# Optimization experiments

Hardware: AMD Instinct MI355X
Metric: run time of the kernel (lower is better)

The kernel has to match this reference:

```python
import jax, jax.numpy as jnp
import numpy as np

EPSILON_BASE = 0.1
N_ITERS = 10


def setup_inputs() -> dict:
    key = jax.random.key(0)
    k1, k2 = jax.random.split(key)
    N, D = 8192, 512
    embeddings = jax.random.normal(k1, (N, D), dtype=jnp.float32)
    target_noise = jax.random.normal(k2, (N, D), dtype=jnp.float32)
    return {"embeddings": embeddings, "target_noise": target_noise}


def _l2_normalize(x, axis=1, eps=1e-12):
    # matches torch.nn.functional.normalize (divide by max(norm, eps))
    norm = jnp.sqrt(jnp.sum(x * x, axis=axis, keepdims=True))
    return x / jnp.maximum(norm, eps)


def _sinkhorn(x, y):
    n, d = x.shape
    # normalize_embeddings=True path
    x = _l2_normalize(x, axis=1)
    y = _l2_normalize(y, axis=1)
    epsilon = EPSILON_BASE * 2.0
    # squared euclidean cost: C[i,j] = ||x_i - y_j||^2  (cdist p=2, squared)
    sq_x = jnp.sum(x * x, axis=1, keepdims=True)          # (n,1)
    sq_y = jnp.sum(y * y, axis=1, keepdims=True)          # (n,1)
    C = jnp.maximum(sq_x + sq_y.T - 2.0 * (x @ y.T), 0.0)  # (n,n)
    log_K = -C / epsilon

    def body(carry, _):
        log_u, log_v = carry
        log_u = -jax.nn.logsumexp(log_K + log_v[None, :], axis=1)
        log_v = -jax.nn.logsumexp(log_K.T + log_u[None, :], axis=1)
        return (log_u, log_v), None

    init = (jnp.zeros(n, dtype=x.dtype), jnp.zeros(n, dtype=y.dtype))
    (log_u, log_v), _ = jax.lax.scan(body, init, None, length=N_ITERS)

    log_P = log_u[:, None] + log_K + log_v[None, :]
    P = jnp.clip(jnp.exp(log_P), 0.0, 1.0)
    distance = jnp.sum(P * C) / n

    # nan/inf fallback: 1 - mean cosine similarity (x, y already unit norm)
    fallback = 1.0 - jnp.mean(jnp.sum(x * y, axis=1))
    bad = jnp.isnan(distance) | jnp.isinf(distance)
    return jnp.where(bad, fallback, distance)


def reference(embeddings, target_noise):
    if embeddings.ndim == 3:
        embeddings = embeddings.reshape(-1, embeddings.shape[-1])
        target_noise = target_noise.reshape(-1, target_noise.shape[-1])
    return _sinkhorn(embeddings, target_noise)
```

## Files before the change

kernel.cpp:

```cpp
#include <hip/hip_runtime.h>
#include <hip/hip_bf16.h>
#include <hip/hip_fp16.h>
#include <stdint.h>

#define NROW 8192
#define DIM  512
#define LN2   0.6931471805599453f
#define TEN_LOG2E 14.426950408889634f

typedef __attribute__((ext_vector_type(8))) short short8;
typedef __attribute__((ext_vector_type(4))) float f32x4;
typedef __attribute__((ext_vector_type(2))) float f32x2;

#define GLL16(gp, lp) __builtin_amdgcn_global_load_lds( \
    (const __attribute__((address_space(1))) void*)(gp), \
    (__attribute__((address_space(3))) void*)(lp), 16, 0, 0)

__device__ __forceinline__ float block_sum256(float v) {
  #pragma unroll
  for (int off = 32; off > 0; off >>= 1) v += __shfl_down(v, off, 64);
  __shared__ float sb[4];
  const int w = threadIdx.x >> 6;
  if ((threadIdx.x & 63) == 0) sb[w] = v;
  __syncthreads();
  return sb[0] + sb[1] + sb[2] + sb[3];
}

__global__ __launch_bounds__(256) void init_kernel(float* __restrict__ colrcp,
                                                   float* __restrict__ diagacc,
                                                   float* __restrict__ distacc) {
  const int g = blockIdx.x * 256 + threadIdx.x;
  colrcp[g] = 1.0f;
  if (g == 0) { diagacc[0] = 0.f; distacc[0] = 0.f; }
}

__global__ __launch_bounds__(256) void normalize_kernel(
    const float* __restrict__ X, const float* __restrict__ Y,
    __hip_bfloat16* __restrict__ Xn, __hip_bfloat16* __restrict__ Yn,
    float* __restrict__ diagacc) {
  const int wave = threadIdx.x >> 6, lane = threadIdx.x & 63;
  float dsum = 0.f;
  #pragma unroll
  for (int rr = 0; rr < 4; rr++) {
    const int row = blockIdx.x * 16 + wave * 4 + rr;
    const float4* xr = (const float4*)(X + (size_t)row * DIM);
    const float4* yr = (const float4*)(Y + (size_t)row * DIM);
    float4 x0 = xr[lane], x1 = xr[lane + 64];
    float4 y0 = yr[lane], y1 = yr[lane + 64];
    float sx = x0.x*x0.x + x0.y*x0.y + x0.z*x0.z + x0.w*x0.w
             + x1.x*x1.x + x1.y*x1.y + x1.z*x1.z + x1.w*x1.w;
    float sy = y0.x*y0.x + y0.y*y0.y + y0.z*y0.z + y0.w*y0.w
             + y1.x*y1.x + y1.y*y1.y + y1.z*y1.z + y1.w*y1.w;
    float sxy = x0.x*y0.x + x0.y*y0.y + x0.z*y0.z + x0.w*y0.w
              + x1.x*y1.x + x1.y*y1.y + x1.z*y1.z + x1.w*y1.w;
    #pragma unroll
    for (int off = 1; off < 64; off <<= 1) {
      sx  += __shfl_xor(sx, off, 64);
      sy  += __shfl_xor(sy, off, 64);
      sxy += __shfl_xor(sxy, off, 64);
    }
    const float rx = 1.0f / fmaxf(sqrtf(sx), 1e-12f);
    const float ry = 1.0f / fmaxf(sqrtf(sy), 1e-12f);
    if (lane == 0) dsum += sxy * rx * ry;
    ushort4 px, py;
    { __hip_bfloat16 b;
      b = __float2bfloat16(x0.x*rx); px.x = *(unsigned short*)&b;
      b = __float2bfloat16(x0.y*rx); px.y = *(unsigned short*)&b;
      b = __float2bfloat16(x0.z*rx); px.z = *(unsigned short*)&b;
      b = __float2bfloat16(x0.w*rx); px.w = *(unsigned short*)&b;
      b = __float2bfloat16(y0.x*ry); py.x = *(unsigned short*)&b;
      b = __float2bfloat16(y0.y*ry); py.y = *(unsigned short*)&b;
      b = __float2bfloat16(y0.z*ry); py.z = *(unsigned short*)&b;
      b = __float2bfloat16(y0.w*ry); py.w = *(unsigned short*)&b;
    }
    ((ushort4*)(Xn + (size_t)row * DIM))[lane] = px;
    ((ushort4*)(Yn + (size_t)row * DIM))[lane] = py;
    { __hip_bfloat16 b;
      b = __float2bfloat16(x1.x*rx); px.x = *(unsigned short*)&b;
      b = __float2bfloat16(x1.y*rx); px.y = *(unsigned short*)&b;
      b = __float2bfloat16(x1.z*rx); px.z = *(unsigned short*)&b;
      b = __float2bfloat16(x1.w*rx); px.w = *(unsigned short*)&b;
      b = __float2bfloat16(y1.x*ry); py.x = *(unsigned short*)&b;
      b = __float2bfloat16(y1.y*ry); py.y = *(unsigned short*)&b;
      b = __float2bfloat16(y1.z*ry); py.z = *(unsigned short*)&b;
      b = __float2bfloat16(y1.w*ry); py.w = *(unsigned short*)&b;
    }
    ((ushort4*)(Xn + (size_t)row * DIM))[lane + 64] = px;
    ((ushort4*)(Yn + (size_t)row * DIM))[lane + 64] = py;
  }
  if (lane == 0) atomicAdd(diagacc, dsum);
}

__global__ __launch_bounds__(256) void gemm_kernel(
    const __hip_bfloat16* __restrict__ A, const __hip_bfloat16* __restrict__ B,
    uint8_t* __restrict__ K, uint8_t* __restrict__ KT) {
  __shared__ int4 smem4[1024];
  short* As = (short*)smem4;
  short* Bs = As + 128 * 32;
  int4* AsI4 = (int4*)As;
  int4* BsI4 = (int4*)Bs;
  const int m0 = blockIdx.y * 128;
  const int n0 = blockIdx.x * 128;
  const int t = threadIdx.x;
  const int wave = t >> 6, lane = t & 63;
  const int wm = (wave & 1) * 64, wn = (wave >> 1) * 64;
  const int fr = lane & 15;
  const int fq = lane >> 4;

  f32x4 acc[4][4];
  #pragma unroll
  for (int i = 0; i < 4; i++)
    #pragma unroll
    for (int j = 0; j < 4; j++) acc[i][j] = (f32x4)0.f;

  const int L0 = t, L1 = t + 256;
  const int ar0 = L0 >> 2, ac0 = L0 & 3;
  const int ar1 = L1 >> 2, ac1 = L1 & 3;
  const int4* Ag0 = (const int4*)A + (size_t)(m0 + ar0) * 64 + ac0;
  const int4* Ag1 = (const int4*)A + (size_t)(m0 + ar1) * 64 + ac1;
  const int4* Bg0 = (const int4*)B + (size_t)(n0 + ar0) * 64 + ac0;
  const int4* Bg1 = (const int4*)B + (size_t)(n0 + ar1) * 64 + ac1;

  for (int kt = 0; kt < 16; ++kt) {
    const int kb = kt * 4;
    __syncthreads();
    GLL16(Ag0 + kb, AsI4 + L0);
    GLL16(Ag1 + kb, AsI4 + L1);
    GLL16(Bg0 + kb, BsI4 + L0);
    GLL16(Bg1 + kb, BsI4 + L1);
    __syncthreads();
    short8 af[4], bfr[4];
    #pragma unroll
    for (int i = 0; i < 4; i++) {
      af[i]  = *(const short8*)&As[(wm + i * 16 + fr) * 32 + fq * 8];
      bfr[i] = *(const short8*)&Bs[(wn + i * 16 + fr) * 32 + fq * 8];
    }
    #pragma unroll
    for (int i = 0; i < 4; i++)
      #pragma unroll
      for (int j = 0; j < 4; j++)
        acc[i][j] = __builtin_amdgcn_mfma_f32_16x16x32_bf16(af[i], bfr[j], acc[i][j], 0, 0, 0);
  }
  __syncthreads();
  uint8_t* tile = (uint8_t*)smem4;
  #pragma unroll
  for (int i = 0; i < 4; i++) {
    #pragma unroll
    for (int j = 0; j < 4; j++) {
      const int R  = wm + i * 16 + fq * 4;
      const int Cc = wn + j * 16 + fr;
      float v0 = exp2f(fminf(acc[i][j][0], 1.0f) * TEN_LOG2E);
      float v1 = exp2f(fminf(acc[i][j][1], 1.0f) * TEN_LOG2E);
      float v2 = exp2f(fminf(acc[i][j][2], 1.0f) * TEN_LOG2E);
      float v3 = exp2f(fminf(acc[i][j][3], 1.0f) * TEN_LOG2E);
      int pk = 0;
      pk = __builtin_amdgcn_cvt_pk_fp8_f32(v0, v1, pk, false);
      pk = __builtin_amdgcn_cvt_pk_fp8_f32(v2, v3, pk, true);
      const int a = Cc * 128 + R;
      *(int*)(tile + (a ^ (((a >> 7) & 7) << 4))) = pk;
      uint8_t* kp = K + (size_t)(m0 + R) * NROW + n0 + Cc;
      kp[0]            = (uint8_t)(pk & 0xff);
      kp[NROW]         = (uint8_t)((pk >> 8) & 0xff);
      kp[2 * NROW]     = (uint8_t)((pk >> 16) & 0xff);
      kp[3 * NROW]     = (uint8_t)((pk >> 24) & 0xff);
    }
  }
  __syncthreads();
  {
    const int r = t >> 1, h = (t & 1) * 64;
    uint8_t* gp = KT + (size_t)(n0 + r) * NROW + m0 + h;
    #pragma unroll
    for (int q = 0; q < 4; q++) {
      const int a = r * 128 + h + q * 16;
      *(int4*)(gp + q * 16) = *(const int4*)(tile + (a ^ (((a >> 7) & 7) << 4)));
    }
  }
}

__global__ __launch_bounds__(256) void pass_kernel(
    const uint8_t* __restrict__ M, const float* __restrict__ w,
    float* __restrict__ out) {
  __shared__ float4 wl[2048];
  const int t = threadIdx.x;
  const int wave = t >> 6, lane = t & 63;
  const int xh = (lane >> 1) & 3;
  const int row0 = blockIdx.x * 16 + wave * 4;
  int4 ka[8], kb[8];
  const int4* Mr0 = (const int4*)(M + (size_t)row0 * NROW);
  #pragma unroll
  for (int c = 0; c < 8; c++) ka[c] = Mr0[c * 64 + lane];
  #pragma unroll
  for (int c = 0; c < 8; c++) {
    const int j = c * 256 + t;
    wl[j ^ ((j >> 3) & 3)] = ((const float4*)w)[j];
  }
  __syncthreads();
  #pragma unroll
  for (int r = 0; r < 4; r++) {
    if (r < 3) {
      const int4* Mn = (const int4*)(M + (size_t)(row0 + r + 1) * NROW);
      #pragma unroll
      for (int c = 0; c < 8; c++) { if (r & 1) ka[c] = Mn[c * 64 + lane]; else kb[c] = Mn[c * 64 + lane]; }
    }
    float acc0 = 0.f, acc1 = 0.f;
    #pragma unroll
    for (int c = 0; c < 8; c++) {
      const int b4 = (c * 64 + lane) * 4;
      const int4 kc = (r & 1) ? kb[c] : ka[c];
      const int* kd = (const int*)&kc;
      #pragma unroll
      for (int q = 0; q < 4; q++) {
        float4 ww = wl[b4 + (q ^ xh)];
        f32x2 lo = __builtin_amdgcn_cvt_pk_f32_fp8(kd[q], false);
        f32x2 hi = __builtin_amdgcn_cvt_pk_f32_fp8(kd[q], true);
        acc0 += lo.x * ww.x + lo.y * ww.y;
        acc1 += hi.x * ww.z + hi.y * ww.w;
      }
    }
    float acc = acc0 + acc1;
    #pragma unroll
    for (int off = 32; off > 0; off >>= 1) acc += __shfl_down(acc, off, 64);
    if (lane == 0) out[row0 + r] = 1.0f / acc;
  }
}

__global__ __launch_bounds__(256) void pass_dist_kernel(
    const uint8_t* __restrict__ KT, const float* __restrict__ u,
    float* __restrict__ distacc) {
  __shared__ float4 wl[2048];
  const int t = threadIdx.x;
  const int wave = t >> 6, lane = t & 63;
  const int xh = (lane >> 1) & 3;
  const int row0 = blockIdx.x * 16 + wave * 4;
  int4 ka[8], kb[8];
  const int4* Mr0 = (const int4*)(KT + (size_t)row0 * NROW);
  #pragma unroll
  for (int c = 0; c < 8; c++) ka[c] = Mr0[c * 64 + lane];
  #pragma unroll
  for (int c = 0; c < 8; c++) {
    const int j = c * 256 + t;
    wl[j ^ ((j >> 3) & 3)] = ((const float4*)u)[j];
  }
  __syncthreads();
  float accd = 0.f;
  #pragma unroll
  for (int r = 0; r < 4; r++) {
    if (r < 3) {
      const int4* Mn = (const int4*)(KT + (size_t)(row0 + r + 1) * NROW);
      #pragma unroll
      for (int c = 0; c < 8; c++) { if (r & 1) ka[c] = Mn[c * 64 + lane]; else kb[c] = Mn[c * 64 + lane]; }
    }
    float acc0 = 0.f, acc1 = 0.f;
    #pragma unroll
    for (int c = 0; c < 8; c++) {
      const int b4 = (c * 64 + lane) * 4;
      const int4 kc = (r & 1) ? kb[c] : ka[c];
      const int* kd = (const int*)&kc;
      #pragma unroll
      for (int q = 0; q < 4; q++) {
        float4 ww = wl[b4 + (q ^ xh)];
        f32x2 lo = __builtin_amdgcn_cvt_pk_f32_fp8(kd[q], false);
        f32x2 hi = __builtin_amdgcn_cvt_pk_f32_fp8(kd[q], true);
        acc0 += lo.x * ww.x + lo.y * ww.y;
        acc1 += hi.x * ww.z + hi.y * ww.w;
      }
    }
    float s = acc0 + acc1;
    #pragma unroll
    for (int off = 1; off < 64; off <<= 1) s += __shfl_xor(s, off, 64);
    const float vj = 1.0f / s;
    #pragma unroll
    for (int c = 0; c < 8; c++) {
      const int b4 = (c * 64 + lane) * 4;
      const int4 kc = (r & 1) ? kb[c] : ka[c];
      const int* kd = (const int*)&kc;
      #pragma unroll
      for (int q = 0; q < 4; q++) {
        float4 ww = wl[b4 + (q ^ xh)];
        f32x2 lo = __builtin_amdgcn_cvt_pk_f32_fp8(kd[q], false);
        f32x2 hi = __builtin_amdgcn_cvt_pk_f32_fp8(kd[q], true);
        float kv[4] = {lo.x, lo.y, hi.x, hi.y};
        float uv[4] = {ww.x, ww.y, ww.z, ww.w};
        #pragma unroll
        for (int e = 0; e < 4; e++) {
          float p = fminf(uv[e] * kv[e] * vj, 1.f);
          float cterm = 2.f - 0.2f * LN2 * __log2f(fmaxf(kv[e], 1e-6f));
          accd += p * cterm;
        }
      }
    }
  }
  float tot = block_sum256(accd);
  if (t == 0) atomicAdd(distacc, tot);
}

__global__ void final_kernel(const float* __restrict__ distacc,
                             const float* __restrict__ diagacc,
                             float* __restrict__ out) {
  if (threadIdx.x == 0 && blockIdx.x == 0) {
    float d = distacc[0] * (1.0f / (float)NROW);
    float fb = 1.0f - diagacc[0] * (1.0f / (float)NROW);
    float v = (isnan(d) || isinf(d)) ? fb : d;
    __hip_bfloat16 b = __float2bfloat16(v);
    unsigned short h = *(unsigned short*)&b;
    ((unsigned int*)out)[0] = ((unsigned int)h << 16) | (unsigned int)h;
  }
}

extern "C" void kernel_launch(void* const* d_in, const int* in_sizes, int n_in,
                              void* d_out, int out_size, void* d_ws, size_t ws_size,
                              hipStream_t stream) {
  (void)in_sizes; (void)n_in; (void)out_size; (void)ws_size;
  const float* X = (const float*)d_in[0];
  const float* Y = (const float*)d_in[1];
  float* out = (float*)d_out;

  char* ws = (char*)d_ws;
  size_t off = 0;
  uint8_t* K  = (uint8_t*)(ws + off); off += (size_t)NROW * NROW;
  uint8_t* KT = (uint8_t*)(ws + off); off += (size_t)NROW * NROW;
  __hip_bfloat16* Xn = (__hip_bfloat16*)(ws + off); off += (size_t)NROW * DIM * 2;
  __hip_bfloat16* Yn = (__hip_bfloat16*)(ws + off); off += (size_t)NROW * DIM * 2;
  float* rowrcp  = (float*)(ws + off); off += NROW * 4;
  float* colrcp  = (float*)(ws + off); off += NROW * 4;
  float* diagacc = (float*)(ws + off); off += 256;
  float* distacc = (float*)(ws + off); off += 256;

  init_kernel<<<32, 256, 0, stream>>>(colrcp, diagacc, distacc);
  normalize_kernel<<<512, 256, 0, stream>>>(X, Y, Xn, Yn, diagacc);
  gemm_kernel<<<dim3(64, 64), 256, 0, stream>>>(Xn, Yn, K, KT);
  for (int it = 0; it < 10; ++it) {
    pass_kernel<<<512, 256, 0, stream>>>(K,  colrcp, rowrcp);
    if (it < 9)
      pass_kernel<<<512, 256, 0, stream>>>(KT, rowrcp, colrcp);
  }
  pass_dist_kernel<<<512, 256, 0, stream>>>(KT, rowrcp, distacc);
  final_kernel<<<1, 64, 0, stream>>>(distacc, diagacc, out);
}
```

Before: 481.0 us.

## Double-buffer LDS tiles in the GEMM kernel to overlap loads with MFMA

The GEMM main loop now ping-pongs between two LDS buffers, using twice the shared memory. It prefetches the next K-slice with global_load_lds while running MFMAs on the current slice, and needs one barrier per iteration instead of two. This is meant to hide global-to-LDS latency behind the matrix math. The larger LDS footprint may lower occupancy, and only the GEMM stage is affected, not the Sinkhorn iterations.

```diff
diff --git a/kernel.cpp b/kernel.cpp
--- a/kernel.cpp
+++ b/kernel.cpp
@@ -94,11 +94,7 @@
 __global__ __launch_bounds__(256) void gemm_kernel(
     const __hip_bfloat16* __restrict__ A, const __hip_bfloat16* __restrict__ B,
     uint8_t* __restrict__ K, uint8_t* __restrict__ KT) {
-  __shared__ int4 smem4[1024];
-  short* As = (short*)smem4;
-  short* Bs = As + 128 * 32;
-  int4* AsI4 = (int4*)As;
-  int4* BsI4 = (int4*)Bs;
+  __shared__ int4 smem4[2048];
   const int m0 = blockIdx.y * 128;
   const int n0 = blockIdx.x * 128;
   const int t = threadIdx.x;
@@ -121,14 +117,30 @@
   const int4* Bg0 = (const int4*)B + (size_t)(n0 + ar0) * 64 + ac0;
   const int4* Bg1 = (const int4*)B + (size_t)(n0 + ar1) * 64 + ac1;
 
+  {
+    int4* AsI4 = smem4;
+    int4* BsI4 = smem4 + 512;
+    GLL16(Ag0, AsI4 + L0);
+    GLL16(Ag1, AsI4 + L1);
+    GLL16(Bg0, BsI4 + L0);
+    GLL16(Bg1, BsI4 + L1);
+  }
+  __syncthreads();
+
+  #pragma unroll 2
   for (int kt = 0; kt < 16; ++kt) {
-    const int kb = kt * 4;
-    __syncthreads();
-    GLL16(Ag0 + kb, AsI4 + L0);
-    GLL16(Ag1 + kb, AsI4 + L1);
-    GLL16(Bg0 + kb, BsI4 + L0);
-    GLL16(Bg1 + kb, BsI4 + L1);
-    __syncthreads();
+    const int cur = kt & 1;
+    if (kt < 15) {
+      const int kb = (kt + 1) * 4;
+      int4* AsN = smem4 + (cur ^ 1) * 1024;
+      int4* BsN = AsN + 512;
+      GLL16(Ag0 + kb, AsN + L0);
+      GLL16(Ag1 + kb, AsN + L1);
+      GLL16(Bg0 + kb, BsN + L0);
+      GLL16(Bg1 + kb, BsN + L1);
+    }
+    const short* As = (const short*)(smem4 + cur * 1024);
+    const short* Bs = As + 128 * 32;
     short8 af[4], bfr[4];
     #pragma unroll
     for (int i = 0; i < 4; i++) {
@@ -140,8 +152,8 @@
       #pragma unroll
       for (int j = 0; j < 4; j++)
         acc[i][j] = __builtin_amdgcn_mfma_f32_16x16x32_bf16(af[i], bfr[j], acc[i][j], 0, 0, 0);
-  }
-  __syncthreads();
+    __syncthreads();
+  }
   uint8_t* tile = (uint8_t*)smem4;
   #pragma unroll
   for (int i = 0; i < 4; i++) {
```

New measurement: 484.5 us. About the same (+0.7%).
